# Kernel tuning notes

Measured on AMD Instinct MI355X. Metric: run time of the kernel, lower is better.

The kernel has to match this reference:

```python
import jax, jax.numpy as jnp
import numpy as np

K = 5
INPLANES = 256
PLANES = 384
M = 4
CM = INPLANES // M  # 64 channels after reduction; also the group count
STRIDE = 1


def setup_inputs() -> dict:
    key = jax.random.key(0)
    ks = jax.random.split(key, 19)

    def w(k, shape, s=0.05):
        return jax.random.normal(k, shape, dtype=jnp.float32) * s

    return {
        "x": jax.random.normal(ks[0], (32, INPLANES, 64, 64), dtype=jnp.float32),
        "conv_w": w(ks[1], (CM, INPLANES)),       # self.conv (1x1)
        "conv_b": w(ks[2], (CM,)),
        "ck_w": w(ks[3], ()),                      # self.conv_k (1->1 1x1 == scalar affine)
        "ck_b": w(ks[4], ()),
        "ck2_w": w(ks[5], ()),                     # self.conv_k2
        "ck2_b": w(ks[6], ()),
        "ckd4_w": w(ks[7], ()),                    # self.conv_k_d4
        "ckd4_b": w(ks[8], ()),
        "kern_w": w(ks[9], (K * K,)),              # self.conv_kernel (1 -> k*k, 1x1)
        "kern_b": w(ks[10], (K * K,)),
        "kern2_w": w(ks[11], (9,)),                # self.conv_kernel2 (1 -> 9)
        "kern2_b": w(ks[12], (9,)),
        "kernd4_w": w(ks[13], (9,)),               # self.conv_kernel_d4 (1 -> 9)
        "kernd4_b": w(ks[14], (9,)),
        "fuse_w": w(ks[15], (PLANES // 3, CM)),    # self.fuse (1x1)
        "fuse_b": w(ks[16], (PLANES // 3,)),
        "fc_w": w(ks[17], (PLANES, PLANES // 3 * 3)),  # self.fuse_channel (1x1)
        "fc_b": w(ks[18], (PLANES,)),
    }


def _depthwise(f, ker, pad, dil):
    # Per-sample depthwise conv: fold batch into channels -> one grouped conv.
    # f: [N, CM, H, W], ker: [N, CM, kh, kw]
    N, Cm, H, W = f.shape
    kh, kw = ker.shape[2], ker.shape[3]
    x = f.reshape(1, N * Cm, H, W)
    wgt = ker.reshape(N * Cm, 1, kh, kw)
    out = jax.lax.conv_general_dilated(
        x, wgt, window_strides=(STRIDE, STRIDE),
        padding=[(pad, pad), (pad, pad)], rhs_dilation=(dil, dil),
        feature_group_count=N * Cm,
        dimension_numbers=('NCHW', 'OIHW', 'NCHW'))
    return out.reshape(N, Cm, out.shape[2], out.shape[3])


def reference(x, conv_w, conv_b, ck_w, ck_b, ck2_w, ck2_b, ckd4_w, ckd4_b,
              kern_w, kern_b, kern2_w, kern2_b, kernd4_w, kernd4_b,
              fuse_w, fuse_b, fc_w, fc_b):
    N = x.shape[0]
    # f = relu(conv(x)), g = relu(conv(avg_pool(x)))
    f = jax.nn.relu(jnp.einsum('nchw,oc->nohw', x, conv_w) + conv_b[None, :, None, None])
    g = jax.nn.relu(jnp.mean(x, axis=(2, 3)) @ conv_w.T + conv_b)  # [N, CM]

    def dyn_kernel(kw, kb, sw, sb, kk):
        # conv_kernel*: scalar g[n,c] -> kk*kk values; conv_k*: scalar affine on top.
        ker = sw * (g[:, :, None] * kw[None, None, :] + kb[None, None, :]) + sb
        return ker.reshape(N, CM, kk, kk)

    k1 = dyn_kernel(kern_w, kern_b, ck_w, ck_b, K)
    k2 = dyn_kernel(kern2_w, kern2_b, ck2_w, ck2_b, 3)
    k3 = dyn_kernel(kernd4_w, kernd4_b, ckd4_w, ckd4_b, 3)

    pad0 = (K - 1) // 2
    o1 = _depthwise(f, k1, pad0, 1)   # k x k, dilation 1
    o2 = _depthwise(f, k2, 2, 2)      # 3x3, dilation 2, pad 2
    o3 = _depthwise(f, k3, 4, 4)      # 3x3, dilation 4, pad 4

    def fuse(o):
        return jnp.einsum('nchw,oc->nohw', o, fuse_w) + fuse_b[None, :, None, None]

    y = jnp.concatenate([fuse(o1), fuse(o2), fuse(o3)], axis=1)
    return jnp.einsum('nchw,oc->nohw', y, fc_w) + fc_b[None, :, None, None]
```

## Files before the change

kernel.cpp:

```cpp
#include <hip/hip_runtime.h>

#define NB   32
#define CIN  256
#define CM   64
#define HWSZ 4096
#define OC   384
#define KTOT 192

typedef __attribute__((ext_vector_type(8))) short bf16x8;
typedef __attribute__((ext_vector_type(4))) float f32x4;

static __device__ __forceinline__ unsigned short f2bf(float v) {
    union { float f; unsigned u; } a; a.f = v;
    unsigned r = a.u + 0x7fffu + ((a.u >> 16) & 1u);
    return (unsigned short)(r >> 16);
}
static __device__ __forceinline__ float bf2f(unsigned short u) {
    union { unsigned u; float f; } a; a.u = ((unsigned)u) << 16;
    return a.f;
}

__global__ void kw_pre(const float* __restrict__ fuse_w, const float* __restrict__ fuse_b,
                       const float* __restrict__ fc_w, const float* __restrict__ fc_b,
                       const float* __restrict__ conv_w,
                       unsigned short* __restrict__ Wb, float* __restrict__ bt,
                       unsigned short* __restrict__ cwb) {
    int k = blockIdx.x;
    int o = threadIdx.x;
    if (k == KTOT) {
        __shared__ float fb[128];
        if (o < 128) fb[o] = fuse_b[o];
        __syncthreads();
        float s = fc_b[o];
        #pragma unroll 4
        for (int q = 0; q < 384; ++q) s += fc_w[o * 384 + q] * fb[q & 127];
        bt[o] = s;
        for (int idx = o; idx < CM * CIN; idx += 384) cwb[idx] = f2bf(conv_w[idx]);
        return;
    }
    int i = k >> 6, c = k & 63;
    __shared__ float fw[128];
    if (o < 128) fw[o] = fuse_w[o * 64 + c];
    __syncthreads();
    float s = 0.f;
    #pragma unroll 8
    for (int j = 0; j < 128; ++j) s += fc_w[o * 384 + i * 128 + j] * fw[j];
    Wb[o * KTOT + k] = f2bf(s);
}

__global__ void k1_mean(const float* __restrict__ x, float* __restrict__ xm) {
    int cin = blockIdx.x, n = blockIdx.y;
    const float* p = x + ((size_t)n * CIN + cin) * HWSZ;
    int t = threadIdx.x;
    float s = 0.f;
    #pragma unroll
    for (int j = 0; j < 4; ++j) {
        float4 v = *(const float4*)(p + j * 1024 + 4 * t);
        s += v.x + v.y + v.z + v.w;
    }
    #pragma unroll
    for (int off = 32; off > 0; off >>= 1) s += __shfl_down(s, off);
    __shared__ float ws[4];
    if ((t & 63) == 0) ws[t >> 6] = s;
    __syncthreads();
    if (t == 0) xm[n * CIN + cin] = (ws[0] + ws[1] + ws[2] + ws[3]) * (1.0f / 4096.0f);
}

__global__ void k2_gk(const float* __restrict__ xm, const float* __restrict__ conv_w,
                      const float* __restrict__ conv_b,
                      const float* ck_w, const float* ck_b, const float* ck2_w, const float* ck2_b,
                      const float* ckd4_w, const float* ckd4_b,
                      const float* kern_w, const float* kern_b,
                      const float* kern2_w, const float* kern2_b,
                      const float* kernd4_w, const float* kernd4_b,
                      float* __restrict__ karr_t) {
    int n = blockIdx.x;
    int c = threadIdx.x;
    __shared__ float xs[CIN];
    for (int i = c; i < CIN; i += 64) xs[i] = xm[n * CIN + i];
    __syncthreads();
    float a = conv_b[c];
    #pragma unroll 8
    for (int i = 0; i < CIN; ++i) a += xs[i] * conv_w[c * CIN + i];
    float g = fmaxf(a, 0.f);
    float* kp = karr_t + (size_t)n * 43 * CM;
    float sw = ck_w[0], sb = ck_b[0];
    #pragma unroll
    for (int i = 0; i < 25; ++i) kp[i * CM + c] = sw * (g * kern_w[i] + kern_b[i]) + sb;
    sw = ck2_w[0]; sb = ck2_b[0];
    #pragma unroll
    for (int i = 0; i < 9; ++i) kp[(25 + i) * CM + c] = sw * (g * kern2_w[i] + kern2_b[i]) + sb;
    sw = ckd4_w[0]; sb = ckd4_b[0];
    #pragma unroll
    for (int i = 0; i < 9; ++i) kp[(34 + i) * CM + c] = sw * (g * kernd4_w[i] + kernd4_b[i]) + sb;
}

__global__ void __launch_bounds__(256) k3_fconv(const float* __restrict__ x,
                                                const unsigned short* __restrict__ cwb,
                                                const float* __restrict__ conv_b,
                                                unsigned short* __restrict__ f_t) {
    __shared__ unsigned short Ab[256 * 40];
    __shared__ unsigned short Bb[64 * 264];
    int pt = blockIdx.x, n = blockIdx.y;
    int p0 = pt * 256;
    int t = threadIdx.x;
    int lane = t & 63, wv = t >> 6;
    int q = lane >> 4, m16 = lane & 15;

    #pragma unroll
    for (int i = 0; i < 8; ++i) {
        int id = t + i * 256;
        int row = id >> 5, seg = id & 31;
        bf16x8 v = *(const bf16x8*)(cwb + row * CIN + seg * 8);
        *(bf16x8*)(&Bb[row * 264 + seg * 8]) = v;
    }

    f32x4 acc[4][4];
    #pragma unroll
    for (int mt = 0; mt < 4; ++mt)
        #pragma unroll
        for (int nt = 0; nt < 4; ++nt)
            #pragma unroll
            for (int r = 0; r < 4; ++r) acc[mt][nt][r] = 0.f;

    const float* xn = x + (size_t)n * CIN * HWSZ;

    for (int kc = 0; kc < 8; ++kc) {
        __syncthreads();
        #pragma unroll
        for (int i = 0; i < 2; ++i) {
            int id = t + i * 256;
            int pg = id & 63, kq = id >> 6;
            int cin = kc * 32 + kq * 4;
            const float* xp = xn + (size_t)cin * HWSZ + p0 + pg * 4;
            float4 r0 = *(const float4*)(xp);
            float4 r1 = *(const float4*)(xp + HWSZ);
            float4 r2 = *(const float4*)(xp + 2 * HWSZ);
            float4 r3 = *(const float4*)(xp + 3 * HWSZ);
            uint2 w;
            w.x = (unsigned)f2bf(r0.x) | ((unsigned)f2bf(r1.x) << 16);
            w.y = (unsigned)f2bf(r2.x) | ((unsigned)f2bf(r3.x) << 16);
            *(uint2*)(&Ab[(pg * 4 + 0) * 40 + kq * 4]) = w;
            w.x = (unsigned)f2bf(r0.y) | ((unsigned)f2bf(r1.y) << 16);
            w.y = (unsigned)f2bf(r2.y) | ((unsigned)f2bf(r3.y) << 16);
            *(uint2*)(&Ab[(pg * 4 + 1) * 40 + kq * 4]) = w;
            w.x = (unsigned)f2bf(r0.z) | ((unsigned)f2bf(r1.z) << 16);
            w.y = (unsigned)f2bf(r2.z) | ((unsigned)f2bf(r3.z) << 16);
            *(uint2*)(&Ab[(pg * 4 + 2) * 40 + kq * 4]) = w;
            w.x = (unsigned)f2bf(r0.w) | ((unsigned)f2bf(r1.w) << 16);
            w.y = (unsigned)f2bf(r2.w) | ((unsigned)f2bf(r3.w) << 16);
            *(uint2*)(&Ab[(pg * 4 + 3) * 40 + kq * 4]) = w;
        }
        __syncthreads();
        bf16x8 af[4], bfr[4];
        #pragma unroll
        for (int mt = 0; mt < 4; ++mt)
            af[mt] = *(const bf16x8*)(&Ab[(wv * 64 + mt * 16 + m16) * 40 + q * 8]);
        #pragma unroll
        for (int nt = 0; nt < 4; ++nt)
            bfr[nt] = *(const bf16x8*)(&Bb[(nt * 16 + m16) * 264 + kc * 32 + q * 8]);
        #pragma unroll
        for (int mt = 0; mt < 4; ++mt)
            #pragma unroll
            for (int nt = 0; nt < 4; ++nt)
                acc[mt][nt] = __builtin_amdgcn_mfma_f32_16x16x32_bf16(af[mt], bfr[nt], acc[mt][nt], 0, 0, 0);
    }

    unsigned short* fo = f_t + (size_t)n * HWSZ * CM;
    #pragma unroll
    for (int nt = 0; nt < 4; ++nt) {
        int ch = nt * 16 + m16;
        float b = conv_b[ch];
        #pragma unroll
        for (int mt = 0; mt < 4; ++mt) {
            int pixb = p0 + wv * 64 + mt * 16 + q * 4;
            #pragma unroll
            for (int r = 0; r < 4; ++r) {
                float v = fmaxf(acc[mt][nt][r] + b, 0.f);
                fo[(size_t)(pixb + r) * CM + ch] = f2bf(v);
            }
        }
    }
}

__global__ void __launch_bounds__(256) k4_dw(const unsigned short* __restrict__ f_t,
                                             const float* __restrict__ karr_t,
                                             unsigned short* __restrict__ o_t) {
    __shared__ unsigned short fl[384 * 72];
    __shared__ float kt[43 * 66];
    int tile = blockIdx.x, n = blockIdx.y;
    int r0 = (tile >> 2) * 8, c0 = (tile & 3) * 16;
    int t = threadIdx.x;

    const unsigned short* fn = f_t + (size_t)n * HWSZ * CM;
    #pragma unroll
    for (int i = 0; i < 12; ++i) {
        int id = t + i * 256;
        int cg = id & 7, pl = id >> 3;
        int lr = pl / 24, lc = pl - lr * 24;
        int gr = r0 + lr - 4, gc = c0 + lc - 4;
        bf16x8 v;
        if ((unsigned)gr < 64u && (unsigned)gc < 64u) {
            v = *(const bf16x8*)(fn + (size_t)(gr * 64 + gc) * CM + cg * 8);
        } else {
            #pragma unroll
            for (int j = 0; j < 8; ++j) v[j] = 0;
        }
        *(bf16x8*)(&fl[pl * 72 + cg * 8]) = v;
    }
    const float* kn = karr_t + (size_t)n * 43 * CM;
    for (int id = t; id < 43 * 64; id += 256) {
        int row = id >> 6, col = id & 63;
        kt[row * 66 + col] = kn[id];
    }
    __syncthreads();

    int cp = t & 31;
    int pg = t >> 5;
    unsigned short* on = o_t + (size_t)n * HWSZ * KTOT;
    for (int pass = 0; pass < 16; ++pass) {
        int pli = pg + pass * 8;
        int row = pli >> 4, col = pli & 15;
        int base = ((row + 4) * 24 + (col + 4)) * 72 + cp * 2;
        float s1e = 0.f, s1o = 0.f, s2e = 0.f, s2o = 0.f, s3e = 0.f, s3o = 0.f;
        #pragma unroll
        for (int ky = 0; ky < 5; ++ky)
            #pragma unroll
            for (int kx = 0; kx < 5; ++kx) {
                unsigned fv = *(const unsigned*)(&fl[base + ((ky - 2) * 24 + (kx - 2)) * 72]);
                float2 tp = *(const float2*)(&kt[(ky * 5 + kx) * 66 + cp * 2]);
                s1e = fmaf(tp.x, bf2f((unsigned short)(fv & 0xffffu)), s1e);
                s1o = fmaf(tp.y, bf2f((unsigned short)(fv >> 16)), s1o);
            }
        #pragma unroll
        for (int ky = 0; ky < 3; ++ky)
            #pragma unroll
            for (int kx = 0; kx < 3; ++kx) {
                unsigned fv = *(const unsigned*)(&fl[base + ((ky * 2 - 2) * 24 + (kx * 2 - 2)) * 72]);
                float2 tp = *(const float2*)(&kt[(25 + ky * 3 + kx) * 66 + cp * 2]);
                s2e = fmaf(tp.x, bf2f((unsigned short)(fv & 0xffffu)), s2e);
                s2o = fmaf(tp.y, bf2f((unsigned short)(fv >> 16)), s2o);
            }
        #pragma unroll
        for (int ky = 0; ky < 3; ++ky)
            #pragma unroll
            for (int kx = 0; kx < 3; ++kx) {
                unsigned fv = *(const unsigned*)(&fl[base + ((ky * 4 - 4) * 24 + (kx * 4 - 4)) * 72]);
                float2 tp = *(const float2*)(&kt[(34 + ky * 3 + kx) * 66 + cp * 2]);
                s3e = fmaf(tp.x, bf2f((unsigned short)(fv & 0xffffu)), s3e);
                s3o = fmaf(tp.y, bf2f((unsigned short)(fv >> 16)), s3o);
            }
        size_t ob = (size_t)((r0 + row) * 64 + (c0 + col)) * KTOT;
        *(unsigned*)(on + ob + cp * 2)       = (unsigned)f2bf(s1e) | ((unsigned)f2bf(s1o) << 16);
        *(unsigned*)(on + ob + 64 + cp * 2)  = (unsigned)f2bf(s2e) | ((unsigned)f2bf(s2o) << 16);
        *(unsigned*)(on + ob + 128 + cp * 2) = (unsigned)f2bf(s3e) | ((unsigned)f2bf(s3o) << 16);
    }
}

__global__ void __launch_bounds__(256) k5_gemm(const unsigned short* __restrict__ o_t,
                                               const unsigned short* __restrict__ Wb,
                                               const float* __restrict__ bt,
                                               float* __restrict__ out) {
    __shared__ unsigned short Ab[128 * 72];
    __shared__ unsigned short Bb[128 * 72];
    __shared__ float bts[128];
    int pt = blockIdx.x, n = blockIdx.y, og = blockIdx.z;
    int p0 = pt * 128, ocb = og * 128;
    int t = threadIdx.x;
    int lane = t & 63, wv = t >> 6;
    int wm = wv >> 1, wn = wv & 1;
    int q = lane >> 4, m16 = lane & 15;
    if (t < 128) bts[t] = bt[ocb + t];

    f32x4 acc[4][4];
    #pragma unroll
    for (int mt = 0; mt < 4; ++mt)
        #pragma unroll
        for (int nt = 0; nt < 4; ++nt)
            #pragma unroll
            for (int r = 0; r < 4; ++r) acc[mt][nt][r] = 0.f;

    const unsigned short* on = o_t + (size_t)n * HWSZ * KTOT + (size_t)p0 * KTOT;

    for (int kc = 0; kc < 3; ++kc) {
        int k0 = kc * 64;
        __syncthreads();
        #pragma unroll
        for (int i = 0; i < 4; ++i) {
            int id = t + i * 256;
            int cg = id & 7, row = id >> 3;
            bf16x8 va = *(const bf16x8*)(Wb + (size_t)(ocb + row) * KTOT + k0 + cg * 8);
            *(bf16x8*)(&Ab[row * 72 + cg * 8]) = va;
            bf16x8 vb = *(const bf16x8*)(on + (size_t)row * KTOT + k0 + cg * 8);
            *(bf16x8*)(&Bb[row * 72 + cg * 8]) = vb;
        }
        __syncthreads();
        #pragma unroll
        for (int ks = 0; ks < 2; ++ks) {
            bf16x8 af[4], bfr[4];
            #pragma unroll
            for (int mt = 0; mt < 4; ++mt)
                af[mt] = *(const bf16x8*)(&Ab[(wm * 64 + mt * 16 + m16) * 72 + ks * 32 + q * 8]);
            #pragma unroll
            for (int nt = 0; nt < 4; ++nt)
                bfr[nt] = *(const bf16x8*)(&Bb[(wn * 64 + nt * 16 + m16) * 72 + ks * 32 + q * 8]);
            #pragma unroll
            for (int mt = 0; mt < 4; ++mt)
                #pragma unroll
                for (int nt = 0; nt < 4; ++nt)
                    acc[mt][nt] = __builtin_amdgcn_mfma_f32_16x16x32_bf16(af[mt], bfr[nt], acc[mt][nt], 0, 0, 0);
        }
    }

    float* outn = out + (size_t)n * OC * HWSZ;
    #pragma unroll
    for (int mt = 0; mt < 4; ++mt) {
        #pragma unroll
        for (int r = 0; r < 4; ++r) {
            int ocl = wm * 64 + mt * 16 + q * 4 + r;
            float b = bts[ocl];
            float* orow = outn + (size_t)(ocb + ocl) * HWSZ + p0 + wn * 64 + m16;
            #pragma unroll
            for (int nt = 0; nt < 4; ++nt)
                orow[nt * 16] = acc[mt][nt][r] + b;
        }
    }
}

extern "C" void kernel_launch(void* const* d_in, const int* in_sizes, int n_in,
                              void* d_out, int out_size, void* d_ws, size_t ws_size,
                              hipStream_t stream) {
    const float* x       = (const float*)d_in[0];
    const float* conv_w  = (const float*)d_in[1];
    const float* conv_b  = (const float*)d_in[2];
    const float* ck_w    = (const float*)d_in[3];
    const float* ck_b    = (const float*)d_in[4];
    const float* ck2_w   = (const float*)d_in[5];
    const float* ck2_b   = (const float*)d_in[6];
    const float* ckd4_w  = (const float*)d_in[7];
    const float* ckd4_b  = (const float*)d_in[8];
    const float* kern_w  = (const float*)d_in[9];
    const float* kern_b  = (const float*)d_in[10];
    const float* kern2_w = (const float*)d_in[11];
    const float* kern2_b = (const float*)d_in[12];
    const float* kernd4_w= (const float*)d_in[13];
    const float* kernd4_b= (const float*)d_in[14];
    const float* fuse_w  = (const float*)d_in[15];
    const float* fuse_b  = (const float*)d_in[16];
    const float* fc_w    = (const float*)d_in[17];
    const float* fc_b    = (const float*)d_in[18];
    float* out = (float*)d_out;

    char* ws = (char*)d_ws;
    float* xm             = (float*)(ws + 0);
    float* karr_t         = (float*)(ws + 32768);
    float* bt             = (float*)(ws + 385024);
    unsigned short* Wb    = (unsigned short*)(ws + 386560);
    unsigned short* cwb   = (unsigned short*)(ws + 534016);
    unsigned short* f_t   = (unsigned short*)(ws + 566784);
    unsigned short* o_t   = (unsigned short*)(ws + 17344000);

    kw_pre<<<dim3(193), dim3(384), 0, stream>>>(fuse_w, fuse_b, fc_w, fc_b, conv_w, Wb, bt, cwb);
    k1_mean<<<dim3(CIN, NB), dim3(256), 0, stream>>>(x, xm);
    k2_gk<<<dim3(NB), dim3(64), 0, stream>>>(xm, conv_w, conv_b,
        ck_w, ck_b, ck2_w, ck2_b, ckd4_w, ckd4_b,
        kern_w, kern_b, kern2_w, kern2_b, kernd4_w, kernd4_b, karr_t);
    k3_fconv<<<dim3(16, NB), dim3(256), 0, stream>>>(x, cwb, conv_b, f_t);
    k4_dw<<<dim3(32, NB), dim3(256), 0, stream>>>(f_t, karr_t, o_t);
    k5_gemm<<<dim3(32, NB, 3), dim3(256), 0, stream>>>(o_t, Wb, bt, out);
}
```

Baseline: 466.2 us.

## Fuse mean into 1x1 conv via atomics and fuse depthwise with fuse GEMM

The spatial mean of x is now accumulated with wave shuffles and atomics inside the first 1x1 conv, which removes the separate full read of x. The depthwise conv kernel and the final channel GEMM are merged into one kernel that keeps the depthwise outputs in shared memory. This avoids writing and re-reading the bf16 intermediate buffer. In exchange it adds atomic contention, a larger shared-memory footprint with 512-thread blocks, and output stores that are less contiguous (16-pixel row segments).

```diff
diff --git a/kernel.cpp b/kernel.cpp
--- a/kernel.cpp
+++ b/kernel.cpp
@@ -24,7 +24,7 @@
                        const float* __restrict__ fc_w, const float* __restrict__ fc_b,
                        const float* __restrict__ conv_w,
                        unsigned short* __restrict__ Wb, float* __restrict__ bt,
-                       unsigned short* __restrict__ cwb) {
+                       unsigned short* __restrict__ cwb, float* __restrict__ xm) {
     int k = blockIdx.x;
     int o = threadIdx.x;
     if (k == KTOT) {
@@ -36,6 +36,7 @@
         for (int q = 0; q < 384; ++q) s += fc_w[o * 384 + q] * fb[q & 127];
         bt[o] = s;
         for (int idx = o; idx < CM * CIN; idx += 384) cwb[idx] = f2bf(conv_w[idx]);
+        for (int idx = o; idx < NB * CIN; idx += 384) xm[idx] = 0.f;
         return;
     }
     int i = k >> 6, c = k & 63;
@@ -48,63 +49,18 @@
     Wb[o * KTOT + k] = f2bf(s);
 }
 
-__global__ void k1_mean(const float* __restrict__ x, float* __restrict__ xm) {
-    int cin = blockIdx.x, n = blockIdx.y;
-    const float* p = x + ((size_t)n * CIN + cin) * HWSZ;
-    int t = threadIdx.x;
-    float s = 0.f;
-    #pragma unroll
-    for (int j = 0; j < 4; ++j) {
-        float4 v = *(const float4*)(p + j * 1024 + 4 * t);
-        s += v.x + v.y + v.z + v.w;
-    }
-    #pragma unroll
-    for (int off = 32; off > 0; off >>= 1) s += __shfl_down(s, off);
-    __shared__ float ws[4];
-    if ((t & 63) == 0) ws[t >> 6] = s;
-    __syncthreads();
-    if (t == 0) xm[n * CIN + cin] = (ws[0] + ws[1] + ws[2] + ws[3]) * (1.0f / 4096.0f);
-}
-
-__global__ void k2_gk(const float* __restrict__ xm, const float* __restrict__ conv_w,
-                      const float* __restrict__ conv_b,
-                      const float* ck_w, const float* ck_b, const float* ck2_w, const float* ck2_b,
-                      const float* ckd4_w, const float* ckd4_b,
-                      const float* kern_w, const float* kern_b,
-                      const float* kern2_w, const float* kern2_b,
-                      const float* kernd4_w, const float* kernd4_b,
-                      float* __restrict__ karr_t) {
-    int n = blockIdx.x;
-    int c = threadIdx.x;
-    __shared__ float xs[CIN];
-    for (int i = c; i < CIN; i += 64) xs[i] = xm[n * CIN + i];
-    __syncthreads();
-    float a = conv_b[c];
-    #pragma unroll 8
-    for (int i = 0; i < CIN; ++i) a += xs[i] * conv_w[c * CIN + i];
-    float g = fmaxf(a, 0.f);
-    float* kp = karr_t + (size_t)n * 43 * CM;
-    float sw = ck_w[0], sb = ck_b[0];
-    #pragma unroll
-    for (int i = 0; i < 25; ++i) kp[i * CM + c] = sw * (g * kern_w[i] + kern_b[i]) + sb;
-    sw = ck2_w[0]; sb = ck2_b[0];
-    #pragma unroll
-    for (int i = 0; i < 9; ++i) kp[(25 + i) * CM + c] = sw * (g * kern2_w[i] + kern2_b[i]) + sb;
-    sw = ckd4_w[0]; sb = ckd4_b[0];
-    #pragma unroll
-    for (int i = 0; i < 9; ++i) kp[(34 + i) * CM + c] = sw * (g * kernd4_w[i] + kernd4_b[i]) + sb;
-}
-
 __global__ void __launch_bounds__(256) k3_fconv(const float* __restrict__ x,
                                                 const unsigned short* __restrict__ cwb,
                                                 const float* __restrict__ conv_b,
-                                                unsigned short* __restrict__ f_t) {
+                                                unsigned short* __restrict__ f_t,
+                                                float* __restrict__ xm) {
     __shared__ unsigned short Ab[256 * 40];
     __shared__ unsigned short Bb[64 * 264];
     int pt = blockIdx.x, n = blockIdx.y;
     int p0 = pt * 256;
     int t = threadIdx.x;
-    int lane = t & 63, wv = t >> 6;
+    int lane = t & 63;
+    int wv = t >> 6;
     int q = lane >> 4, m16 = lane & 15;
 
     #pragma unroll
@@ -130,9 +86,9 @@
         #pragma unroll
         for (int i = 0; i < 2; ++i) {
             int id = t + i * 256;
-            int pg = id & 63, kq = id >> 6;
-            int cin = kc * 32 + kq * 4;
-            const float* xp = xn + (size_t)cin * HWSZ + p0 + pg * 4;
+            int kq = id & 7, pg = id >> 3;
+            int cin0 = kc * 32 + kq * 4;
+            const float* xp = xn + (size_t)cin0 * HWSZ + p0 + pg * 4;
             float4 r0 = *(const float4*)(xp);
             float4 r1 = *(const float4*)(xp + HWSZ);
             float4 r2 = *(const float4*)(xp + 2 * HWSZ);
@@ -150,6 +106,24 @@
             w.x = (unsigned)f2bf(r0.w) | ((unsigned)f2bf(r1.w) << 16);
             w.y = (unsigned)f2bf(r2.w) | ((unsigned)f2bf(r3.w) << 16);
             *(uint2*)(&Ab[(pg * 4 + 3) * 40 + kq * 4]) = w;
+            float s0 = r0.x + r0.y + r0.z + r0.w;
+            float s1 = r1.x + r1.y + r1.z + r1.w;
+            float s2 = r2.x + r2.y + r2.z + r2.w;
+            float s3 = r3.x + r3.y + r3.z + r3.w;
+            #pragma unroll
+            for (int off = 8; off < 64; off <<= 1) {
+                s0 += __shfl_xor(s0, off);
+                s1 += __shfl_xor(s1, off);
+                s2 += __shfl_xor(s2, off);
+                s3 += __shfl_xor(s3, off);
+            }
+            if (lane < 8) {
+                float* xp2 = xm + n * CIN + kc * 32 + lane * 4;
+                atomicAdd(xp2 + 0, s0);
+                atomicAdd(xp2 + 1, s1);
+                atomicAdd(xp2 + 2, s2);
+                atomicAdd(xp2 + 3, s3);
+            }
         }
         __syncthreads();
         bf16x8 af[4], bfr[4];
@@ -183,19 +157,52 @@
     }
 }
 
-__global__ void __launch_bounds__(256) k4_dw(const unsigned short* __restrict__ f_t,
-                                             const float* __restrict__ karr_t,
-                                             unsigned short* __restrict__ o_t) {
+__global__ void k2_gk(const float* __restrict__ xm, const float* __restrict__ conv_w,
+                      const float* __restrict__ conv_b,
+                      const float* ck_w, const float* ck_b, const float* ck2_w, const float* ck2_b,
+                      const float* ckd4_w, const float* ckd4_b,
+                      const float* kern_w, const float* kern_b,
+                      const float* kern2_w, const float* kern2_b,
+                      const float* kernd4_w, const float* kernd4_b,
+                      float* __restrict__ karr_t) {
+    int n = blockIdx.x;
+    int c = threadIdx.x;
+    __shared__ float xs[CIN];
+    for (int i = c; i < CIN; i += 64) xs[i] = xm[n * CIN + i] * (1.0f / 4096.0f);
+    __syncthreads();
+    float a = conv_b[c];
+    #pragma unroll 8
+    for (int i = 0; i < CIN; ++i) a += xs[i] * conv_w[c * CIN + i];
+    float g = fmaxf(a, 0.f);
+    float* kp = karr_t + (size_t)n * 43 * CM;
+    float sw = ck_w[0], sb = ck_b[0];
+    #pragma unroll
+    for (int i = 0; i < 25; ++i) kp[i * CM + c] = sw * (g * kern_w[i] + kern_b[i]) + sb;
+    sw = ck2_w[0]; sb = ck2_b[0];
+    #pragma unroll
+    for (int i = 0; i < 9; ++i) kp[(25 + i) * CM + c] = sw * (g * kern2_w[i] + kern2_b[i]) + sb;
+    sw = ckd4_w[0]; sb = ckd4_b[0];
+    #pragma unroll
+    for (int i = 0; i < 9; ++i) kp[(34 + i) * CM + c] = sw * (g * kernd4_w[i] + kernd4_b[i]) + sb;
+}
+
+__global__ void __launch_bounds__(512, 2) k45_dwgemm(const unsigned short* __restrict__ f_t,
+                                                     const float* __restrict__ karr_t,
+                                                     const unsigned short* __restrict__ Wb,
+                                                     const float* __restrict__ bt,
+                                                     float* __restrict__ out) {
     __shared__ unsigned short fl[384 * 72];
-    __shared__ float kt[43 * 66];
+    __shared__ unsigned short ot[128 * 200];
+    __shared__ float bts[128];
     int tile = blockIdx.x, n = blockIdx.y;
     int r0 = (tile >> 2) * 8, c0 = (tile & 3) * 16;
     int t = threadIdx.x;
+    int lane = t & 63, wv = t >> 6;
 
     const unsigned short* fn = f_t + (size_t)n * HWSZ * CM;
     #pragma unroll
-    for (int i = 0; i < 12; ++i) {
-        int id = t + i * 256;
+    for (int i = 0; i < 6; ++i) {
+        int id = t + i * 512;
         int cg = id & 7, pl = id >> 3;
         int lr = pl / 24, lc = pl - lr * 24;
         int gr = r0 + lr - 4, gc = c0 + lc - 4;
@@ -208,18 +215,20 @@
         }
         *(bf16x8*)(&fl[pl * 72 + cg * 8]) = v;
     }
-    const float* kn = karr_t + (size_t)n * 43 * CM;
-    for (int id = t; id < 43 * 64; id += 256) {
-        int row = id >> 6, col = id & 63;
-        kt[row * 66 + col] = kn[id];
-    }
-    __syncthreads();
-
     int cp = t & 31;
     int pg = t >> 5;
-    unsigned short* on = o_t + (size_t)n * HWSZ * KTOT;
-    for (int pass = 0; pass < 16; ++pass) {
-        int pli = pg + pass * 8;
+    const float* kn = karr_t + (size_t)n * 43 * CM + cp * 2;
+    float2 t1[25], t2[9], t3[9];
+    #pragma unroll
+    for (int i = 0; i < 25; ++i) t1[i] = *(const float2*)(kn + i * CM);
+    #pragma unroll
+    for (int i = 0; i < 9; ++i) t2[i] = *(const float2*)(kn + (25 + i) * CM);
+    #pragma unroll
+    for (int i = 0; i < 9; ++i) t3[i] = *(const float2*)(kn + (34 + i) * CM);
+    __syncthreads();
+
+    for (int pass = 0; pass < 8; ++pass) {
+        int pli = pg + pass * 16;
         int row = pli >> 4, col = pli & 15;
         int base = ((row + 4) * 24 + (col + 4)) * 72 + cp * 2;
         float s1e = 0.f, s1o = 0.f, s2e = 0.f, s2o = 0.f, s3e = 0.f, s3o = 0.f;
@@ -228,7 +237,7 @@
             #pragma unroll
             for (int kx = 0; kx < 5; ++kx) {
                 unsigned fv = *(const unsigned*)(&fl[base + ((ky - 2) * 24 + (kx - 2)) * 72]);
-                float2 tp = *(const float2*)(&kt[(ky * 5 + kx) * 66 + cp * 2]);
+                float2 tp = t1[ky * 5 + kx];
                 s1e = fmaf(tp.x, bf2f((unsigned short)(fv & 0xffffu)), s1e);
                 s1o = fmaf(tp.y, bf2f((unsigned short)(fv >> 16)), s1o);
             }
@@ -237,7 +246,7 @@
             #pragma unroll
             for (int kx = 0; kx < 3; ++kx) {
                 unsigned fv = *(const unsigned*)(&fl[base + ((ky * 2 - 2) * 24 + (kx * 2 - 2)) * 72]);
-                float2 tp = *(const float2*)(&kt[(25 + ky * 3 + kx) * 66 + cp * 2]);
+                float2 tp = t2[ky * 3 + kx];
                 s2e = fmaf(tp.x, bf2f((unsigned short)(fv & 0xffffu)), s2e);
                 s2o = fmaf(tp.y, bf2f((unsigned short)(fv >> 16)), s2o);
             }
@@ -246,83 +255,66 @@
             #pragma unroll
             for (int kx = 0; kx < 3; ++kx) {
                 unsigned fv = *(const unsigned*)(&fl[base + ((ky * 4 - 4) * 24 + (kx * 4 - 4)) * 72]);
-                float2 tp = *(const float2*)(&kt[(34 + ky * 3 + kx) * 66 + cp * 2]);
+                float2 tp = t3[ky * 3 + kx];
                 s3e = fmaf(tp.x, bf2f((unsigned short)(fv & 0xffffu)), s3e);
                 s3o = fmaf(tp.y, bf2f((unsigned short)(fv >> 16)), s3o);
             }
-        size_t ob = (size_t)((r0 + row) * 64 + (c0 + col)) * KTOT;
-        *(unsigned*)(on + ob + cp * 2)       = (unsigned)f2bf(s1e) | ((unsigned)f2bf(s1o) << 16);
-        *(unsigned*)(on + ob + 64 + cp * 2)  = (unsigned)f2bf(s2e) | ((unsigned)f2bf(s2o) << 16);
-        *(unsigned*)(on + ob + 128 + cp * 2) = (unsigned)f2bf(s3e) | ((unsigned)f2bf(s3o) << 16);
-    }
-}
-
-__global__ void __launch_bounds__(256) k5_gemm(const unsigned short* __restrict__ o_t,
-                                               const unsigned short* __restrict__ Wb,
-                                               const float* __restrict__ bt,
-                                               float* __restrict__ out) {
-    __shared__ unsigned short Ab[128 * 72];
-    __shared__ unsigned short Bb[128 * 72];
-    __shared__ float bts[128];
-    int pt = blockIdx.x, n = blockIdx.y, og = blockIdx.z;
-    int p0 = pt * 128, ocb = og * 128;
-    int t = threadIdx.x;
-    int lane = t & 63, wv = t >> 6;
-    int wm = wv >> 1, wn = wv & 1;
+        unsigned short* ob = &ot[pli * 200];
+        *(unsigned*)(ob + cp * 2)       = (unsigned)f2bf(s1e) | ((unsigned)f2bf(s1o) << 16);
+        *(unsigned*)(ob + 64 + cp * 2)  = (unsigned)f2bf(s2e) | ((unsigned)f2bf(s2o) << 16);
+        *(unsigned*)(ob + 128 + cp * 2) = (unsigned)f2bf(s3e) | ((unsigned)f2bf(s3o) << 16);
+    }
+
+    unsigned short* wbs = fl;
+    int wrow = t >> 2, wqk = t & 3;
+    int wm = wv & 3, wn = wv >> 2;
     int q = lane >> 4, m16 = lane & 15;
-    if (t < 128) bts[t] = bt[ocb + t];
-
-    f32x4 acc[4][4];
-    #pragma unroll
-    for (int mt = 0; mt < 4; ++mt)
-        #pragma unroll
-        for (int nt = 0; nt < 4; ++nt)
-            #pragma unroll
-            for (int r = 0; r < 4; ++r) acc[mt][nt][r] = 0.f;
-
-    const unsigned short* on = o_t + (size_t)n * HWSZ * KTOT + (size_t)p0 * KTOT;
-
-    for (int kc = 0; kc < 3; ++kc) {
-        int k0 = kc * 64;
-        __syncthreads();
-        #pragma unroll
-        for (int i = 0; i < 4; ++i) {
-            int id = t + i * 256;
-            int cg = id & 7, row = id >> 3;
-            bf16x8 va = *(const bf16x8*)(Wb + (size_t)(ocb + row) * KTOT + k0 + cg * 8);
-            *(bf16x8*)(&Ab[row * 72 + cg * 8]) = va;
-            bf16x8 vb = *(const bf16x8*)(on + (size_t)row * KTOT + k0 + cg * 8);
-            *(bf16x8*)(&Bb[row * 72 + cg * 8]) = vb;
-        }
-        __syncthreads();
-        #pragma unroll
-        for (int ks = 0; ks < 2; ++ks) {
-            bf16x8 af[4], bfr[4];
-            #pragma unroll
-            for (int mt = 0; mt < 4; ++mt)
-                af[mt] = *(const bf16x8*)(&Ab[(wm * 64 + mt * 16 + m16) * 72 + ks * 32 + q * 8]);
+    float* outn0 = out + (size_t)n * OC * HWSZ;
+    for (int ocg = 0; ocg < 3; ++ocg) {
+        __syncthreads();
+        if (t < 128) bts[t] = bt[ocg * 128 + t];
+        #pragma unroll
+        for (int j = 0; j < 6; ++j) {
+            bf16x8 v = *(const bf16x8*)(Wb + (size_t)(ocg * 128 + wrow) * KTOT + wqk * 48 + j * 8);
+            *(bf16x8*)(&wbs[wrow * 200 + wqk * 48 + j * 8]) = v;
+        }
+        __syncthreads();
+        f32x4 acc[2][4];
+        #pragma unroll
+        for (int mt = 0; mt < 2; ++mt)
             #pragma unroll
             for (int nt = 0; nt < 4; ++nt)
-                bfr[nt] = *(const bf16x8*)(&Bb[(wn * 64 + nt * 16 + m16) * 72 + ks * 32 + q * 8]);
-            #pragma unroll
-            for (int mt = 0; mt < 4; ++mt)
+                #pragma unroll
+                for (int r = 0; r < 4; ++r) acc[mt][nt][r] = 0.f;
+        #pragma unroll
+        for (int ks = 0; ks < 6; ++ks) {
+            bf16x8 af[2], bfr[4];
+            #pragma unroll
+            for (int mt = 0; mt < 2; ++mt)
+                af[mt] = *(const bf16x8*)(&wbs[(wm * 32 + mt * 16 + m16) * 200 + ks * 32 + q * 8]);
+            #pragma unroll
+            for (int nt = 0; nt < 4; ++nt)
+                bfr[nt] = *(const bf16x8*)(&ot[(wn * 64 + nt * 16 + m16) * 200 + ks * 32 + q * 8]);
+            #pragma unroll
+            for (int mt = 0; mt < 2; ++mt)
                 #pragma unroll
                 for (int nt = 0; nt < 4; ++nt)
                     acc[mt][nt] = __builtin_amdgcn_mfma_f32_16x16x32_bf16(af[mt], bfr[nt], acc[mt][nt], 0, 0, 0);
         }
-    }
-
-    float* outn = out + (size_t)n * OC * HWSZ;
-    #pragma unroll
-    for (int mt = 0; mt < 4; ++mt) {
-        #pragma unroll
-        for (int r = 0; r < 4; ++r) {
-            int ocl = wm * 64 + mt * 16 + q * 4 + r;
-            float b = bts[ocl];
-            float* orow = outn + (size_t)(ocb + ocl) * HWSZ + p0 + wn * 64 + m16;
-            #pragma unroll
-            for (int nt = 0; nt < 4; ++nt)
-                orow[nt * 16] = acc[mt][nt][r] + b;
+        float* outn = outn0 + (size_t)(ocg * 128) * HWSZ;
+        #pragma unroll
+        for (int mt = 0; mt < 2; ++mt) {
+            #pragma unroll
+            for (int r = 0; r < 4; ++r) {
+                int ocl = wm * 32 + mt * 16 + q * 4 + r;
+                float b = bts[ocl];
+                #pragma unroll
+                for (int nt = 0; nt < 4; ++nt) {
+                    int pl = wn * 64 + nt * 16 + m16;
+                    int pr = pl >> 4, pc = pl & 15;
+                    outn[(size_t)ocl * HWSZ + (r0 + pr) * 64 + c0 + pc] = acc[mt][nt][r] + b;
+                }
+            }
         }
     }
 }
@@ -358,14 +350,11 @@
     unsigned short* Wb    = (unsigned short*)(ws + 386560);
     unsigned short* cwb   = (unsigned short*)(ws + 534016);
     unsigned short* f_t   = (unsigned short*)(ws + 566784);
-    unsigned short* o_t   = (unsigned short*)(ws + 17344000);
-
-    kw_pre<<<dim3(193), dim3(384), 0, stream>>>(fuse_w, fuse_b, fc_w, fc_b, conv_w, Wb, bt, cwb);
-    k1_mean<<<dim3(CIN, NB), dim3(256), 0, stream>>>(x, xm);
+
+    kw_pre<<<dim3(193), dim3(384), 0, stream>>>(fuse_w, fuse_b, fc_w, fc_b, conv_w, Wb, bt, cwb, xm);
+    k3_fconv<<<dim3(16, NB), dim3(256), 0, stream>>>(x, cwb, conv_b, f_t, xm);
     k2_gk<<<dim3(NB), dim3(64), 0, stream>>>(xm, conv_w, conv_b,
         ck_w, ck_b, ck2_w, ck2_b, ckd4_w, ckd4_b,
         kern_w, kern_b, kern2_w, kern2_b, kernd4_w, kernd4_b, karr_t);
-    k3_fconv<<<dim3(16, NB), dim3(256), 0, stream>>>(x, cwb, conv_b, f_t);
-    k4_dw<<<dim3(32, NB), dim3(256), 0, stream>>>(f_t, karr_t, o_t);
-    k5_gemm<<<dim3(32, NB, 3), dim3(256), 0, stream>>>(o_t, Wb, bt, out);
-}
+    k45_dwgemm<<<dim3(32, NB), dim3(512), 0, stream>>>(f_t, karr_t, Wb, bt, out);
+}
```

Measured after the change: 434.5 us. -6.8%, faster.
